# Performance work log

Hardware: AMD Instinct MI355X
Metric: run time of the kernel (lower is better)

## Reference

```python
import jax, jax.numpy as jnp
import numpy as np

N = 50000      # nodes
E = 800000     # edges
IN = 128       # in_channels
H = 64         # hidden (= edge_dim)
OUT = 64       # out_channels
BN_EPS = 1e-5


def _bn(h, gamma, beta):
    # BatchNorm1d in training mode: per-feature batch statistics
    mu = h.mean(axis=0)
    var = h.var(axis=0)
    return gamma * (h - mu) * jax.lax.rsqrt(var + BN_EPS) + beta


def _gine_layer(x, src, dst, edge_attr, We, be, W1, b1, g, bb, W2, b2):
    # edge_attr projected to node feature dim: [E, d_in]
    ea = edge_attr @ We.T + be
    # message: relu(x_j + lin(edge_attr)); x_j = x[src]
    m = jax.nn.relu(x[src] + ea)
    # scatter-add aggregate at destination nodes
    agg = jax.ops.segment_sum(m, dst, num_segments=x.shape[0])
    # (1 + eps) * x_r with eps = 0
    out = agg + x
    # MLP: Linear -> BN -> ReLU -> Linear
    h = jax.nn.relu(_bn(out @ W1.T + b1, g, bb))
    return h @ W2.T + b2


def setup_inputs() -> dict:
    key = jax.random.key(0)
    ks = jax.random.split(key, 12)

    def glorot(k, shape):
        return jax.random.normal(k, shape, jnp.float32) / np.float32(np.sqrt(shape[1]))

    return {
        "x": jax.random.normal(ks[0], (N, IN), jnp.float32),
        "edge_index": jax.random.randint(ks[1], (2, E), 0, N, jnp.int64),
        "edge_attr": jax.random.normal(ks[2], (E, H), jnp.float32),
        # layer 0
        "We0": glorot(ks[3], (IN, H)), "be0": jnp.zeros((IN,), jnp.float32),
        "W1_0": glorot(ks[4], (H, IN)), "b1_0": jnp.zeros((H,), jnp.float32),
        "g0": jnp.ones((H,), jnp.float32), "bb0": jnp.zeros((H,), jnp.float32),
        "W2_0": glorot(ks[5], (H, H)), "b2_0": jnp.zeros((H,), jnp.float32),
        # layer 1
        "We1": glorot(ks[6], (H, H)), "be1": jnp.zeros((H,), jnp.float32),
        "W1_1": glorot(ks[7], (H, H)), "b1_1": jnp.zeros((H,), jnp.float32),
        "g1": jnp.ones((H,), jnp.float32), "bb1": jnp.zeros((H,), jnp.float32),
        "W2_1": glorot(ks[8], (OUT, H)), "b2_1": jnp.zeros((OUT,), jnp.float32),
    }


def reference(x, edge_index, edge_attr,
              We0, be0, W1_0, b1_0, g0, bb0, W2_0, b2_0,
              We1, be1, W1_1, b1_1, g1, bb1, W2_1, b2_1):
    src, dst = edge_index[0], edge_index[1]
    h = _gine_layer(x, src, dst, edge_attr, We0, be0, W1_0, b1_0, g0, bb0, W2_0, b2_0)
    h = jax.nn.relu(h)  # dropout p=0.0 -> identity
    return _gine_layer(h, src, dst, edge_attr, We1, be1, W1_1, b1_1, g1, bb1, W2_1, b2_1)
```

## Files before the change

### kernel.cpp

```cpp
#include <hip/hip_runtime.h>
#include <hip/hip_bf16.h>


typedef short bhalf4 __attribute__((ext_vector_type(4)));
typedef short short8 __attribute__((ext_vector_type(8)));
typedef float f32x4 __attribute__((ext_vector_type(4)));
typedef float f32x2 __attribute__((ext_vector_type(2)));

__device__ __forceinline__ short f2bf(float x) {
    unsigned u = __float_as_uint(x);
    unsigned r = (u + 0x7fffu + ((u >> 16) & 1u)) >> 16;
    return (short)r;
}
__device__ __forceinline__ float bf2f(unsigned short u) {
    return __uint_as_float(((unsigned)u) << 16);
}

__global__ __launch_bounds__(256) void hist_kernel(
    const int* __restrict__ ei, int* __restrict__ cnt, int E)
{
    int e = blockIdx.x * 256 + threadIdx.x;
    if (e < E) atomicAdd(&cnt[ei[E + e]], 1);
}

__global__ __launch_bounds__(1024) void scan_kernel(
    const int* __restrict__ cnt, int* __restrict__ offs,
    int* __restrict__ cursor, int N)
{
    __shared__ int wsum[16];
    __shared__ int chunk_base;
    int tid = threadIdx.x;
    int lane = tid & 63, wid = tid >> 6;
    if (tid == 0) chunk_base = 0;
    __syncthreads();
    for (int start = 0; start < N; start += 1024) {
        int i = start + tid;
        int v = (i < N) ? cnt[i] : 0;
        int s = v;
#pragma unroll
        for (int d = 1; d < 64; d <<= 1) {
            int t = __shfl_up(s, d);
            if (lane >= d) s += t;
        }
        if (lane == 63) wsum[wid] = s;
        __syncthreads();
        int wbase = 0;
        for (int w = 0; w < wid; ++w) wbase += wsum[w];
        int excl = chunk_base + wbase + s - v;
        if (i < N) { offs[i] = excl; cursor[i] = excl; }
        int tot = 0;
        for (int w = 0; w < 16; ++w) tot += wsum[w];
        __syncthreads();
        if (tid == 0) chunk_base += tot;
        __syncthreads();
    }
    if (threadIdx.x == 0) offs[N] = chunk_base;
}

__global__ __launch_bounds__(256) void scatter_kernel(
    const int* __restrict__ ei, int* __restrict__ cursor,
    int* __restrict__ inv, int E)
{
    int e = blockIdx.x * 256 + threadIdx.x;
    if (e >= E) return;
    int d = ei[E + e];
    int pos = atomicAdd(&cursor[d], 1);
    inv[e] = pos;
}

__global__ __launch_bounds__(256) void xcast_kernel(
    const float* __restrict__ x, unsigned short* __restrict__ xb, int total)
{
    for (int i = blockIdx.x * 256 + threadIdx.x; i < total; i += gridDim.x * 256)
        xb[i] = (unsigned short)f2bf(x[i]);
}

template<int DF>
__global__ __launch_bounds__(256) void edgem_kernel(
    const unsigned short* __restrict__ xb,
    const int*    __restrict__ ei,
    const float*  __restrict__ eattr,
    const short*  __restrict__ WB,
    const float*  __restrict__ be,
    const int*    __restrict__ inv,
    unsigned short* __restrict__ pbuf,
    int E)
{
    constexpr int FC = DF / 16;
    const int wave = threadIdx.x >> 6;
    const int lane = threadIdx.x & 63;
    const int ebase = (blockIdx.x * 4 + wave) * 16;
    if (ebase >= E) return;
    const int g = lane >> 4, c = lane & 15;

    int ce = ebase + c;
    bool cv = ce < E;
    int ces = cv ? ce : (E - 1);
    int se = ei[ces];
    int sp = cv ? inv[ces] : -1;

    const float* ar = eattr + (size_t)ces * 64 + g * 8;
    f32x4 a0 = *(const f32x4*)(ar);
    f32x4 a1 = *(const f32x4*)(ar + 4);
    f32x4 a2 = *(const f32x4*)(ar + 32);
    f32x4 a3 = *(const f32x4*)(ar + 36);

    bhalf4 xv[FC];
    const unsigned short* xr = xb + (size_t)se * DF + g * 4;
#pragma unroll
    for (int fc = 0; fc < FC; ++fc)
        xv[fc] = *(const bhalf4*)(xr + fc * 16);
    __builtin_amdgcn_sched_barrier(0);

    short8 bfr0, bfr1;
    bfr0[0]=f2bf(a0[0]); bfr0[1]=f2bf(a0[1]); bfr0[2]=f2bf(a0[2]); bfr0[3]=f2bf(a0[3]);
    bfr0[4]=f2bf(a1[0]); bfr0[5]=f2bf(a1[1]); bfr0[6]=f2bf(a1[2]); bfr0[7]=f2bf(a1[3]);
    bfr1[0]=f2bf(a2[0]); bfr1[1]=f2bf(a2[1]); bfr1[2]=f2bf(a2[2]); bfr1[3]=f2bf(a2[3]);
    bfr1[4]=f2bf(a3[0]); bfr1[5]=f2bf(a3[1]); bfr1[6]=f2bf(a3[2]); bfr1[7]=f2bf(a3[3]);

#pragma unroll
    for (int fc = 0; fc < FC; ++fc) {
        const short* aw = WB + (size_t)(fc * 16 + c) * 64 + g * 8;
        short8 aw0 = *(const short8*)(aw);
        short8 aw1 = *(const short8*)(aw + 32);
        f32x4 acc = {0.f, 0.f, 0.f, 0.f};
        acc = __builtin_amdgcn_mfma_f32_16x16x32_bf16(aw0, bfr0, acc, 0, 0, 0);
        acc = __builtin_amdgcn_mfma_f32_16x16x32_bf16(aw1, bfr1, acc, 0, 0, 0);

        f32x4 bev = *(const f32x4*)(be + fc * 16 + g * 4);
        bhalf4 outp;
#pragma unroll
        for (int r = 0; r < 4; ++r) {
            float v = acc[r] + bev[r] + bf2f((unsigned short)xv[fc][r]);
            outp[r] = f2bf(fmaxf(v, 0.f));
        }
        if (sp >= 0)
            *(bhalf4*)(pbuf + (size_t)sp * DF + fc * 16 + g * 4) = outp;
    }
}

__global__ __launch_bounds__(256) void gathersum0_kernel(
    const unsigned short* __restrict__ pbuf,
    const int* __restrict__ offs,
    const float* __restrict__ x,
    unsigned short* __restrict__ sb, int N)
{
    int wid = threadIdx.x >> 6, lane = threadIdx.x & 63;
    int n = blockIdx.x * 4 + wid;
    if (n >= N) return;
    f32x2 xx = *(const f32x2*)(x + (size_t)n * 128 + 2 * lane);
    float s0 = xx[0], s1 = xx[1];
    int i0 = offs[n], i1 = offs[n + 1];
    const unsigned int* p = (const unsigned int*)(pbuf + (size_t)i0 * 128) + lane;
    int cnt = i1 - i0;
    int i = 0;
    for (; i + 3 < cnt; i += 4) {
        unsigned int v0 = p[0], v1 = p[64], v2 = p[128], v3 = p[192];
        s0 += bf2f((unsigned short)v0) + bf2f((unsigned short)v1)
            + bf2f((unsigned short)v2) + bf2f((unsigned short)v3);
        s1 += bf2f((unsigned short)(v0 >> 16)) + bf2f((unsigned short)(v1 >> 16))
            + bf2f((unsigned short)(v2 >> 16)) + bf2f((unsigned short)(v3 >> 16));
        p += 256;
    }
    for (; i < cnt; ++i) {
        unsigned int v = p[0];
        s0 += bf2f((unsigned short)v);
        s1 += bf2f((unsigned short)(v >> 16));
        p += 64;
    }
    unsigned int packed = (unsigned int)(unsigned short)f2bf(s0)
                        | ((unsigned int)(unsigned short)f2bf(s1) << 16);
    *(unsigned int*)(sb + (size_t)n * 128 + 2 * lane) = packed;
}

__global__ __launch_bounds__(256) void gathersum1_kernel(
    const unsigned short* __restrict__ pbuf,
    const int* __restrict__ offs,
    const float* __restrict__ y0, unsigned short* __restrict__ sb, int N)
{
    int wid = threadIdx.x >> 6, lane = threadIdx.x & 63;
    int n = blockIdx.x * 4 + wid;
    if (n >= N) return;
    float s = y0[(size_t)n * 64 + lane];
    int i0 = offs[n], i1 = offs[n + 1];
    const unsigned short* p = pbuf + (size_t)i0 * 64 + lane;
    int cnt = i1 - i0;
    int i = 0;
    for (; i + 3 < cnt; i += 4) {
        s += bf2f(p[0]) + bf2f(p[64]) + bf2f(p[128]) + bf2f(p[192]);
        p += 256;
    }
    for (; i < cnt; ++i) { s += bf2f(p[0]); p += 64; }
    sb[(size_t)n * 64 + lane] = (unsigned short)f2bf(s);
}

template<int DIN>
__global__ __launch_bounds__(256) void ngemm_kernel(
    const unsigned short* __restrict__ A,
    const short* __restrict__ W, const float* __restrict__ b,
    float* __restrict__ out, int N)
{
    constexpr int KK = DIN / 32;
    const int wave = threadIdx.x >> 6;
    const int lane = threadIdx.x & 63;
    const int nbase = (blockIdx.x * 4 + wave) * 16;
    if (nbase >= N) return;
    const int g = lane >> 4, c = lane & 15;

    int rowc = nbase + c; if (rowc >= N) rowc = N - 1;
    const unsigned short* arow = A + (size_t)rowc * DIN + g * 8;
    short8 afr[KK];
#pragma unroll
    for (int kk = 0; kk < KK; ++kk)
        afr[kk] = *(const short8*)(arow + kk * 32);

#pragma unroll
    for (int cc = 0; cc < 4; ++cc) {
        const float bev = b[cc * 16 + c];
        f32x4 acc = {bev, bev, bev, bev};
#pragma unroll
        for (int kk = 0; kk < KK; ++kk) {
            short8 bw = *(const short8*)(W + (size_t)(cc * 16 + c) * DIN + kk * 32 + g * 8);
            acc = __builtin_amdgcn_mfma_f32_16x16x32_bf16(afr[kk], bw, acc, 0, 0, 0);
        }
#pragma unroll
        for (int r = 0; r < 4; ++r) {
            int row = nbase + g * 4 + r;
            if (row < N) out[(size_t)row * 64 + cc * 16 + c] = acc[r];
        }
    }
}

__global__ __launch_bounds__(256) void ngemm_bn_kernel(
    const float* __restrict__ t, const float* __restrict__ scsh,
    const short* __restrict__ W2, const float* __restrict__ b2,
    float* __restrict__ out, unsigned short* __restrict__ outb,
    int N, int relu_out)
{
    const int wave = threadIdx.x >> 6;
    const int lane = threadIdx.x & 63;
    const int nbase = (blockIdx.x * 4 + wave) * 16;
    if (nbase >= N) return;
    const int g = lane >> 4, c = lane & 15;

    int rowc = nbase + c; if (rowc >= N) rowc = N - 1;
    const float* trow = t + (size_t)rowc * 64 + g * 8;

    short8 afr[2];
#pragma unroll
    for (int kk = 0; kk < 2; ++kk) {
        f32x4 q0 = *(const f32x4*)(trow + kk * 32);
        f32x4 q1 = *(const f32x4*)(trow + kk * 32 + 4);
        const int kbase = kk * 32 + g * 8;
        f32x4 sc0 = *(const f32x4*)(scsh + kbase);
        f32x4 sc1 = *(const f32x4*)(scsh + kbase + 4);
        f32x4 sh0 = *(const f32x4*)(scsh + 64 + kbase);
        f32x4 sh1 = *(const f32x4*)(scsh + 64 + kbase + 4);
#pragma unroll
        for (int j = 0; j < 4; ++j) {
            afr[kk][j]     = f2bf(fmaxf(q0[j] * sc0[j] + sh0[j], 0.f));
            afr[kk][j + 4] = f2bf(fmaxf(q1[j] * sc1[j] + sh1[j], 0.f));
        }
    }

#pragma unroll
    for (int cc = 0; cc < 4; ++cc) {
        const float bev = b2[cc * 16 + c];
        f32x4 acc = {bev, bev, bev, bev};
#pragma unroll
        for (int kk = 0; kk < 2; ++kk) {
            short8 bw = *(const short8*)(W2 + (size_t)(cc * 16 + c) * 64 + kk * 32 + g * 8);
            acc = __builtin_amdgcn_mfma_f32_16x16x32_bf16(afr[kk], bw, acc, 0, 0, 0);
        }
#pragma unroll
        for (int r = 0; r < 4; ++r) {
            int row = nbase + g * 4 + r;
            if (row < N) {
                float v = acc[r];
                if (relu_out) {
                    v = fmaxf(v, 0.f);
                    outb[(size_t)row * 64 + cc * 16 + c] = (unsigned short)f2bf(v);
                }
                out[(size_t)row * 64 + cc * 16 + c] = v;
            }
        }
    }
}

__global__ __launch_bounds__(256) void bnstats_kernel(
    const float* __restrict__ t, float* __restrict__ sums, int total)
{
    int tid = threadIdx.x;
    float s = 0.f, s2 = 0.f;
    for (int i = blockIdx.x * 256 + tid; i < total; i += gridDim.x * 256) {
        float v = t[i];
        s += v; s2 += v * v;
    }
    __shared__ float ls[256], ls2[256];
    ls[tid] = s; ls2[tid] = s2;
    __syncthreads();
    if (tid < 64) {
        s  = ls[tid]  + ls[tid + 64]  + ls[tid + 128]  + ls[tid + 192];
        s2 = ls2[tid] + ls2[tid + 64] + ls2[tid + 128] + ls2[tid + 192];
        atomicAdd(&sums[tid], s);
        atomicAdd(&sums[64 + tid], s2);
    }
}

__global__ void bnfinal_kernel(const float* __restrict__ sums,
                               const float* __restrict__ g,
                               const float* __restrict__ bb,
                               float* __restrict__ scsh, float invN)
{
    int f = threadIdx.x;
    float mean = sums[f] * invN;
    float var  = sums[64 + f] * invN - mean * mean;
    float sc = g[f] * rsqrtf(var + 1e-5f);
    scsh[f] = sc;
    scsh[64 + f] = bb[f] - mean * sc;
}

__global__ __launch_bounds__(256) void prep_kernel(
    const float* __restrict__ We0, const float* __restrict__ W1_0,
    const float* __restrict__ We1, const float* __restrict__ W1_1,
    const float* __restrict__ W2_0, const float* __restrict__ W2_1,
    short* __restrict__ WeB0, short* __restrict__ W1B0,
    short* __restrict__ WeB1, short* __restrict__ W1B1,
    short* __restrict__ W2B0, short* __restrict__ W2B1)
{
    int i = blockIdx.x * 256 + threadIdx.x;
    if (i < 128 * 64) WeB0[i] = f2bf(We0[i]);
    if (i < 64 * 128) W1B0[i] = f2bf(W1_0[i]);
    if (i < 64 * 64) {
        WeB1[i] = f2bf(We1[i]);
        W1B1[i] = f2bf(W1_1[i]);
        W2B0[i] = f2bf(W2_0[i]);
        W2B1[i] = f2bf(W2_1[i]);
    }
}

extern "C" void kernel_launch(void* const* d_in, const int* in_sizes, int n_in,
                              void* d_out, int out_size, void* d_ws, size_t ws_size,
                              hipStream_t stream)
{
    (void)n_in; (void)out_size; (void)ws_size;
    const float* x     = (const float*)d_in[0];
    const int*   ei    = (const int*)d_in[1];
    const float* eattr = (const float*)d_in[2];
    const float* We0   = (const float*)d_in[3];
    const float* be0   = (const float*)d_in[4];
    const float* W1_0  = (const float*)d_in[5];
    const float* b1_0  = (const float*)d_in[6];
    const float* g0    = (const float*)d_in[7];
    const float* bb0   = (const float*)d_in[8];
    const float* W2_0  = (const float*)d_in[9];
    const float* b2_0  = (const float*)d_in[10];
    const float* We1   = (const float*)d_in[11];
    const float* be1   = (const float*)d_in[12];
    const float* W1_1  = (const float*)d_in[13];
    const float* b1_1  = (const float*)d_in[14];
    const float* g1    = (const float*)d_in[15];
    const float* bb1   = (const float*)d_in[16];
    const float* W2_1  = (const float*)d_in[17];
    const float* b2_1  = (const float*)d_in[18];
    float* out = (float*)d_out;

    const int N = in_sizes[0] / 128;
    const int E = in_sizes[2] / 64;

    char* ws = (char*)d_ws;
    size_t o = 0;
    auto alloc = [&](size_t bytes) { char* p = ws + o; o = (o + bytes + 255) & ~(size_t)255; return p; };
    unsigned short* pbuf = (unsigned short*)alloc((size_t)E * 128 * 2);
    float* tbuf   = (float*)alloc((size_t)N * 64 * 4);
    float* y0     = (float*)alloc((size_t)N * 64 * 4);
    unsigned short* xb = (unsigned short*)alloc((size_t)N * 128 * 2);
    unsigned short* yb = (unsigned short*)alloc((size_t)N * 64 * 2);
    short* WeB0   = (short*)alloc(128 * 64 * 2);
    short* W1B0   = (short*)alloc(64 * 128 * 2);
    short* WeB1   = (short*)alloc(64 * 64 * 2);
    short* W1B1   = (short*)alloc(64 * 64 * 2);
    short* W2B0   = (short*)alloc(64 * 64 * 2);
    short* W2B1   = (short*)alloc(64 * 64 * 2);
    float* stats  = (float*)alloc(512 * 4);
    int*   cnt    = (int*)alloc((size_t)N * 4);
    int*   offs   = (int*)alloc((size_t)(N + 1) * 4);
    int*   inv    = (int*)alloc((size_t)E * 4);
    float* sum0  = stats;
    float* scsh0 = stats + 128;
    float* sum1  = stats + 256;
    float* scsh1 = stats + 384;
    unsigned short* sb0 = xb;
    unsigned short* sb1 = yb;

    (void)hipMemsetAsync(stats, 0, 512 * 4, stream);
    (void)hipMemsetAsync(cnt, 0, (size_t)N * 4, stream);
    prep_kernel<<<64, 256, 0, stream>>>(We0, W1_0, We1, W1_1, W2_0, W2_1,
                                        WeB0, W1B0, WeB1, W1B1, W2B0, W2B1);
    xcast_kernel<<<2048, 256, 0, stream>>>(x, xb, N * 128);

    const int eb256 = (E + 255) / 256;

    hist_kernel<<<eb256, 256, 0, stream>>>(ei, cnt, E);
    scan_kernel<<<1, 1024, 0, stream>>>(cnt, offs, cnt, N);
    scatter_kernel<<<eb256, 256, 0, stream>>>(ei, cnt, inv, E);

    const int edge_blocks = ((E + 15) / 16 + 3) / 4;
    const int n4_blocks   = (N + 3) / 4;
    const int nt_blocks   = ((N + 15) / 16 + 3) / 4;

    edgem_kernel<128><<<edge_blocks, 256, 0, stream>>>(
        xb, ei, eattr, WeB0, be0, inv, pbuf, E);
    gathersum0_kernel<<<n4_blocks, 256, 0, stream>>>(pbuf, offs, x, sb0, N);
    ngemm_kernel<128><<<nt_blocks, 256, 0, stream>>>(sb0, W1B0, b1_0, tbuf, N);
    bnstats_kernel<<<256, 256, 0, stream>>>(tbuf, sum0, N * 64);
    bnfinal_kernel<<<1, 64, 0, stream>>>(sum0, g0, bb0, scsh0, 1.0f / N);
    ngemm_bn_kernel<<<nt_blocks, 256, 0, stream>>>(
        tbuf, scsh0, W2B0, b2_0, y0, yb, N, 1);

    edgem_kernel<64><<<edge_blocks, 256, 0, stream>>>(
        yb, ei, eattr, WeB1, be1, inv, pbuf, E);
    gathersum1_kernel<<<n4_blocks, 256, 0, stream>>>(pbuf, offs, y0, sb1, N);
    ngemm_kernel<64><<<nt_blocks, 256, 0, stream>>>(sb1, W1B1, b1_1, tbuf, N);
    bnstats_kernel<<<256, 256, 0, stream>>>(tbuf, sum1, N * 64);
    bnfinal_kernel<<<1, 64, 0, stream>>>(sum1, g1, bb1, scsh1, 1.0f / N);
    ngemm_bn_kernel<<<nt_blocks, 256, 0, stream>>>(
        tbuf, scsh1, W2B1, b2_1, out, yb, N, 0);
}
```

Measured before the change: 647.0 us.

## Stage edge attributes and gathered rows through LDS for coalesced row accesses

The edge-message kernel now loads edge attributes and gathered source-node rows cooperatively into per-wave shared-memory tiles, with lanes covering contiguous row segments in wide vector loads. The MFMA operands and x values are then read from LDS, and results are written back into the tile. A final pass stores whole 16-byte chunks per row into the permuted output buffer. The aim is to replace scattered 8-byte per-lane global gathers and stores with wider, more coalesced row transactions, at the cost of extra LDS traffic, wait barriers and shared memory that may limit occupancy.

```diff
diff --git a/kernel.cpp b/kernel.cpp
--- a/kernel.cpp
+++ b/kernel.cpp
@@ -86,37 +86,50 @@
     unsigned short* __restrict__ pbuf,
     int E)
 {
-    constexpr int FC = DF / 16;
+    constexpr int FC  = DF / 16;
+    constexpr int SA  = 72;
+    constexpr int SX  = DF + 8;
+    constexpr int LPR = DF / 8;
+    constexpr int RPI = 64 / LPR;
+    constexpr int NI  = 16 / RPI;
+    __shared__ short attr[4][16][SA];
+    __shared__ short xm[4][16][SX];
     const int wave = threadIdx.x >> 6;
     const int lane = threadIdx.x & 63;
     const int ebase = (blockIdx.x * 4 + wave) * 16;
     if (ebase >= E) return;
     const int g = lane >> 4, c = lane & 15;
-
-    int ce = ebase + c;
-    bool cv = ce < E;
-    int ces = cv ? ce : (E - 1);
-    int se = ei[ces];
-    int sp = cv ? inv[ces] : -1;
-
-    const float* ar = eattr + (size_t)ces * 64 + g * 8;
-    f32x4 a0 = *(const f32x4*)(ar);
-    f32x4 a1 = *(const f32x4*)(ar + 4);
-    f32x4 a2 = *(const f32x4*)(ar + 32);
-    f32x4 a3 = *(const f32x4*)(ar + 36);
-
-    bhalf4 xv[FC];
-    const unsigned short* xr = xb + (size_t)se * DF + g * 4;
-#pragma unroll
-    for (int fc = 0; fc < FC; ++fc)
-        xv[fc] = *(const bhalf4*)(xr + fc * 16);
+    short* at = &attr[wave][0][0];
+    short* xt = &xm[wave][0][0];
+
+    {
+        int r = lane >> 2, q = lane & 3;
+        int e = ebase + r;
+        const float* src = eattr + (size_t)((e < E) ? e : (E - 1)) * 64;
+#pragma unroll
+        for (int i = 0; i < 4; ++i) {
+            f32x4 v = *(const f32x4*)(src + q * 4 + i * 16);
+            bhalf4 b;
+            b[0] = f2bf(v[0]); b[1] = f2bf(v[1]); b[2] = f2bf(v[2]); b[3] = f2bf(v[3]);
+            *(bhalf4*)(at + r * SA + i * 16 + q * 4) = b;
+        }
+    }
+    {
+#pragma unroll
+        for (int i = 0; i < NI; ++i) {
+            int r = i * RPI + lane / LPR;
+            int q = lane % LPR;
+            int e = ebase + r;
+            int se = ei[(e < E) ? e : (E - 1)];
+            short8 v = *(const short8*)(xb + (size_t)se * DF + q * 8);
+            *(short8*)(xt + r * SX + q * 8) = v;
+        }
+    }
+    asm volatile("s_waitcnt lgkmcnt(0)" ::: "memory");
     __builtin_amdgcn_sched_barrier(0);
 
-    short8 bfr0, bfr1;
-    bfr0[0]=f2bf(a0[0]); bfr0[1]=f2bf(a0[1]); bfr0[2]=f2bf(a0[2]); bfr0[3]=f2bf(a0[3]);
-    bfr0[4]=f2bf(a1[0]); bfr0[5]=f2bf(a1[1]); bfr0[6]=f2bf(a1[2]); bfr0[7]=f2bf(a1[3]);
-    bfr1[0]=f2bf(a2[0]); bfr1[1]=f2bf(a2[1]); bfr1[2]=f2bf(a2[2]); bfr1[3]=f2bf(a2[3]);
-    bfr1[4]=f2bf(a3[0]); bfr1[5]=f2bf(a3[1]); bfr1[6]=f2bf(a3[2]); bfr1[7]=f2bf(a3[3]);
+    short8 bfr0 = *(const short8*)(at + c * SA + g * 8);
+    short8 bfr1 = *(const short8*)(at + c * SA + 32 + g * 8);
 
 #pragma unroll
     for (int fc = 0; fc < FC; ++fc) {
@@ -128,14 +141,31 @@
         acc = __builtin_amdgcn_mfma_f32_16x16x32_bf16(aw1, bfr1, acc, 0, 0, 0);
 
         f32x4 bev = *(const f32x4*)(be + fc * 16 + g * 4);
-        bhalf4 outp;
+        short* slot = xt + c * SX + fc * 16 + g * 4;
+        bhalf4 xv = *(const bhalf4*)(slot);
+        bhalf4 mo;
 #pragma unroll
         for (int r = 0; r < 4; ++r) {
-            float v = acc[r] + bev[r] + bf2f((unsigned short)xv[fc][r]);
-            outp[r] = f2bf(fmaxf(v, 0.f));
-        }
-        if (sp >= 0)
-            *(bhalf4*)(pbuf + (size_t)sp * DF + fc * 16 + g * 4) = outp;
+            float v = acc[r] + bev[r] + bf2f((unsigned short)xv[r]);
+            mo[r] = f2bf(fmaxf(v, 0.f));
+        }
+        *(bhalf4*)(slot) = mo;
+    }
+    asm volatile("s_waitcnt lgkmcnt(0)" ::: "memory");
+    __builtin_amdgcn_sched_barrier(0);
+
+    {
+#pragma unroll
+        for (int i = 0; i < NI; ++i) {
+            int r = i * RPI + lane / LPR;
+            int q = lane % LPR;
+            int e = ebase + r;
+            short8 v = *(const short8*)(xt + r * SX + q * 8);
+            if (e < E) {
+                int sp = inv[e];
+                *(short8*)(pbuf + (size_t)sp * DF + q * 8) = v;
+            }
+        }
     }
 }
 
```

After: 530.9 us, median of 2. 1.22x faster.

## Stage edge messages through swizzled LDS for full-row 16-byte gather and scatter

Applied to the files above, without the earlier changes.

The edge-message kernel now gathers source-node rows with 16-byte loads into a per-wave, XOR-swizzled shared-memory tile, so consecutive lanes cover one contiguous row. It computes the messages in place in LDS and writes them back to the permuted buffer as contiguous 16-byte stores per row. Before, each lane loaded and stored scattered 8-byte pieces in the MFMA output layout. The cost is extra LDS traffic, explicit lgkmcnt waits, and more registers for the per-row indices, with no cross-wave barrier because each wave owns its own tile.

```diff
diff --git a/kernel.cpp b/kernel.cpp
--- a/kernel.cpp
+++ b/kernel.cpp
@@ -86,30 +86,40 @@
     unsigned short* __restrict__ pbuf,
     int E)
 {
-    constexpr int FC = DF / 16;
+    constexpr int FC  = DF / 16;
+    constexpr int LPR = DF / 8;
+    constexpr int RPI = 64 / LPR;
+    constexpr int NI  = 16 / RPI;
+    __shared__ short xm[4][16][DF];
     const int wave = threadIdx.x >> 6;
     const int lane = threadIdx.x & 63;
     const int ebase = (blockIdx.x * 4 + wave) * 16;
     if (ebase >= E) return;
     const int g = lane >> 4, c = lane & 15;
+    short* xt = &xm[wave][0][0];
 
     int ce = ebase + c;
-    bool cv = ce < E;
-    int ces = cv ? ce : (E - 1);
-    int se = ei[ces];
-    int sp = cv ? inv[ces] : -1;
-
+    int ces = (ce < E) ? ce : (E - 1);
     const float* ar = eattr + (size_t)ces * 64 + g * 8;
     f32x4 a0 = *(const f32x4*)(ar);
     f32x4 a1 = *(const f32x4*)(ar + 4);
     f32x4 a2 = *(const f32x4*)(ar + 32);
     f32x4 a3 = *(const f32x4*)(ar + 36);
 
-    bhalf4 xv[FC];
-    const unsigned short* xr = xb + (size_t)se * DF + g * 4;
-#pragma unroll
-    for (int fc = 0; fc < FC; ++fc)
-        xv[fc] = *(const bhalf4*)(xr + fc * 16);
+    int srow[NI], sq[NI], spos[NI];
+#pragma unroll
+    for (int i = 0; i < NI; ++i) {
+        int r = i * RPI + lane / LPR;
+        int q = lane % LPR;
+        int e = ebase + r;
+        bool v = e < E;
+        int es = v ? e : (E - 1);
+        srow[i] = r; sq[i] = q;
+        spos[i] = v ? inv[es] : -1;
+        int se = ei[es];
+        short8 xv = *(const short8*)(xb + (size_t)se * DF + q * 8);
+        *(short8*)(xt + r * DF + (q ^ (r & 7)) * 8) = xv;
+    }
     __builtin_amdgcn_sched_barrier(0);
 
     short8 bfr0, bfr1;
@@ -118,24 +128,45 @@
     bfr1[0]=f2bf(a2[0]); bfr1[1]=f2bf(a2[1]); bfr1[2]=f2bf(a2[2]); bfr1[3]=f2bf(a2[3]);
     bfr1[4]=f2bf(a3[0]); bfr1[5]=f2bf(a3[1]); bfr1[6]=f2bf(a3[2]); bfr1[7]=f2bf(a3[3]);
 
+    f32x4 acc[FC];
 #pragma unroll
     for (int fc = 0; fc < FC; ++fc) {
         const short* aw = WB + (size_t)(fc * 16 + c) * 64 + g * 8;
         short8 aw0 = *(const short8*)(aw);
         short8 aw1 = *(const short8*)(aw + 32);
-        f32x4 acc = {0.f, 0.f, 0.f, 0.f};
-        acc = __builtin_amdgcn_mfma_f32_16x16x32_bf16(aw0, bfr0, acc, 0, 0, 0);
-        acc = __builtin_amdgcn_mfma_f32_16x16x32_bf16(aw1, bfr1, acc, 0, 0, 0);
-
+        f32x4 a = {0.f, 0.f, 0.f, 0.f};
+        a = __builtin_amdgcn_mfma_f32_16x16x32_bf16(aw0, bfr0, a, 0, 0, 0);
+        a = __builtin_amdgcn_mfma_f32_16x16x32_bf16(aw1, bfr1, a, 0, 0, 0);
+        acc[fc] = a;
+    }
+
+    asm volatile("s_waitcnt lgkmcnt(0)" ::: "memory");
+    __builtin_amdgcn_sched_barrier(0);
+
+#pragma unroll
+    for (int fc = 0; fc < FC; ++fc) {
+        int slot = (fc * 2 + (g >> 1)) ^ (c & 7);
+        short* addr = xt + c * DF + slot * 8 + (g & 1) * 4;
         f32x4 bev = *(const f32x4*)(be + fc * 16 + g * 4);
-        bhalf4 outp;
+        bhalf4 xv = *(const bhalf4*)(addr);
+        bhalf4 mo;
 #pragma unroll
         for (int r = 0; r < 4; ++r) {
-            float v = acc[r] + bev[r] + bf2f((unsigned short)xv[fc][r]);
-            outp[r] = f2bf(fmaxf(v, 0.f));
-        }
-        if (sp >= 0)
-            *(bhalf4*)(pbuf + (size_t)sp * DF + fc * 16 + g * 4) = outp;
+            float v = acc[fc][r] + bev[r] + bf2f((unsigned short)xv[r]);
+            mo[r] = f2bf(fmaxf(v, 0.f));
+        }
+        *(bhalf4*)(addr) = mo;
+    }
+
+    asm volatile("s_waitcnt lgkmcnt(0)" ::: "memory");
+    __builtin_amdgcn_sched_barrier(0);
+
+#pragma unroll
+    for (int i = 0; i < NI; ++i) {
+        int r = srow[i], q = sq[i];
+        short8 v = *(const short8*)(xt + r * DF + (q ^ (r & 7)) * 8);
+        if (spos[i] >= 0)
+            *(short8*)(pbuf + (size_t)spos[i] * DF + q * 8) = v;
     }
 }
 
```

Measured after the change: 567.6 us. 1.14x faster.
